# Performance work log

Measured on AMD Instinct MI355X. Metric: run time of the kernel, lower is better.

## Reference

```python
import jax, jax.numpy as jnp
import numpy as np

H, RANK, BATCH, T = 1024, 4, 128, 256


def setup_inputs() -> dict:
    key = jax.random.key(0)
    ks = jax.random.split(key, 6)
    s = 1.0 / np.sqrt(H)  # glorot-ish scale for params
    return {
        "x": jax.random.normal(ks[0], (BATCH, T, H), jnp.float32),
        "h0": jnp.zeros((BATCH, H), jnp.float32),
        "d": jax.random.normal(ks[1], (H,), jnp.float32) * s,
        "L": jax.random.normal(ks[2], (H, RANK), jnp.float32) * s,
        "R": jax.random.normal(ks[3], (RANK, H), jnp.float32) * s,
        "B": jax.random.normal(ks[4], (H, H), jnp.float32) * s,
    }


def reference(x, h0, d, L, R, B):
    # Input projection B.T @ x_t for all steps at once (one big GEMM):
    # (B.T @ x)_i = sum_j B[j,i] x[j]  ->  x @ B
    xB = jnp.einsum("bth,hk->btk", x, B)  # [batch, T, H]

    def step(h, u):  # h: [batch, H], u: [batch, H]
        # diagonal + rank-4 low-rank update: d*h + L @ (R @ h) + B.T @ x
        low_rank = (h @ R.T) @ L.T  # [batch, H]
        h = jnp.tanh(d * h + low_rank + u)
        return h, h

    _, hs = jax.lax.scan(step, h0, jnp.swapaxes(xB, 0, 1))  # hs: [T, batch, H]
    return jnp.swapaxes(hs, 0, 1)  # [batch, T, H]
```

## Files before the change

### kernel.cpp

```cpp
#include <hip/hip_runtime.h>
#include <hip/hip_bf16.h>

#define H_DIM  1024
#define RANK_  4
#define BATCH_ 128
#define TSTEPS 256
#define M_DIM  (BATCH_ * TSTEPS)

typedef __bf16 bf16x8 __attribute__((ext_vector_type(8)));
typedef float  floatx4 __attribute__((ext_vector_type(4)));
typedef unsigned short ushortx8 __attribute__((ext_vector_type(8)));

__device__ __forceinline__ unsigned short f2bf(float f) {
    unsigned u = __float_as_uint(f);
    u += 0x7FFFu + ((u >> 16) & 1u);
    return (unsigned short)(u >> 16);
}

#define NXB ((M_DIM * H_DIM) / (256 * 8))

__global__ __launch_bounds__(256) void cvt_fused_kernel(const float* __restrict__ x,
                                                        unsigned short* __restrict__ xb,
                                                        const float* __restrict__ B,
                                                        unsigned short* __restrict__ Bt) {
    __shared__ float tl[32][33];
    const int bid = blockIdx.x;
    if (bid < NXB) {
        size_t i = ((size_t)bid * 256 + threadIdx.x) * 8;
        float4 v0 = *(const float4*)(x + i);
        float4 v1 = *(const float4*)(x + i + 4);
        ushortx8 o;
        o[0] = f2bf(v0.x); o[1] = f2bf(v0.y); o[2] = f2bf(v0.z); o[3] = f2bf(v0.w);
        o[4] = f2bf(v1.x); o[5] = f2bf(v1.y); o[6] = f2bf(v1.z); o[7] = f2bf(v1.w);
        *(ushortx8*)(xb + i) = o;
    } else {
        const int t = bid - NXB;
        int tx = threadIdx.x & 31, ty = threadIdx.x >> 5;
        int k0 = (t >> 5) * 32, n0 = (t & 31) * 32;
#pragma unroll
        for (int j = 0; j < 4; ++j)
            tl[ty + 8 * j][tx] = B[(size_t)(k0 + ty + 8 * j) * H_DIM + n0 + tx];
        __syncthreads();
#pragma unroll
        for (int j = 0; j < 4; ++j)
            Bt[(size_t)(n0 + ty + 8 * j) * H_DIM + k0 + tx] = f2bf(tl[tx][ty + 8 * j]);
    }
}


#define BM 256
#define BN 256
#define BKK 64
#define KTILES (H_DIM / BKK)

#define GLD(srcptr, dstptr)                                          \
    __builtin_amdgcn_global_load_lds(                                \
        (const __attribute__((address_space(1))) void*)(srcptr),     \
        (__attribute__((address_space(3))) void*)(dstptr), 16, 0, 0)

#define STAGE_A(buf, hf, kt) do {                                                     \
    GLD(aS0 + (size_t)(hf) * (128 * H_DIM) + (kt) * BKK, &lds[buf][0][hf][dst0]);     \
    GLD(aS1 + (size_t)(hf) * (128 * H_DIM) + (kt) * BKK, &lds[buf][0][hf][dst1]);     \
} while (0)

#define STAGE_B(buf, hf, kt) do {                                                     \
    GLD(bS0 + (size_t)(hf) * (128 * H_DIM) + (kt) * BKK, &lds[buf][1][hf][dst0]);     \
    GLD(bS1 + (size_t)(hf) * (128 * H_DIM) + (kt) * BKK, &lds[buf][1][hf][dst1]);     \
} while (0)

#define MFMA_PHASE(q)                                                                                         \
    _Pragma("unroll")                                                                                         \
    for (int fc = 0; fc < 4; ++fc) {                                                                          \
        acc[2*(q)][fc]   = __builtin_amdgcn_mfma_f32_16x16x32_bf16(a00, bfr[fc][0], acc[2*(q)][fc], 0, 0, 0);   \
        acc[2*(q)][fc]   = __builtin_amdgcn_mfma_f32_16x16x32_bf16(a01, bfr[fc][1], acc[2*(q)][fc], 0, 0, 0);   \
        acc[2*(q)+1][fc] = __builtin_amdgcn_mfma_f32_16x16x32_bf16(a10, bfr[fc][0], acc[2*(q)+1][fc], 0, 0, 0); \
        acc[2*(q)+1][fc] = __builtin_amdgcn_mfma_f32_16x16x32_bf16(a11, bfr[fc][1], acc[2*(q)+1][fc], 0, 0, 0); \
    }

#define PHASE(q, STAGE_STMT, TAIL_STMT) {                                      \
        bf16x8 a00 = *(const bf16x8*)(Ah + (2*(q))     * 1024 + aRow + cs0);   \
        bf16x8 a01 = *(const bf16x8*)(Ah + (2*(q))     * 1024 + aRow + cs1);   \
        bf16x8 a10 = *(const bf16x8*)(Ah + (2*(q) + 1) * 1024 + aRow + cs0);   \
        bf16x8 a11 = *(const bf16x8*)(Ah + (2*(q) + 1) * 1024 + aRow + cs1);   \
        STAGE_STMT;                                                            \
        __builtin_amdgcn_s_barrier();                                          \
        asm volatile("s_waitcnt lgkmcnt(0)" ::: "memory");                     \
        __builtin_amdgcn_s_setprio(1);                                         \
        MFMA_PHASE(q);                                                         \
        __builtin_amdgcn_s_setprio(0);                                         \
        TAIL_STMT;                                                             \
        __builtin_amdgcn_s_barrier();                                          \
    }

__global__ __launch_bounds__(512, 2) void gemm_bf16_256(const unsigned short* __restrict__ A,
                                                        const unsigned short* __restrict__ Bt,
                                                        float* __restrict__ C) {
    __shared__ unsigned short lds[2][2][2][8192];

    const int tid = threadIdx.x;
    const int l   = tid & 63;
    const int w   = tid >> 6;
    const int wr  = w >> 2;
    const int wc  = w & 3;

    const int bid = blockIdx.x;
    const int lt  = (bid & 7) * 64 + (bid >> 3);
    const int m0  = (lt >> 2) * BM;
    const int n0  = (lt & 3)  * BN;

    const int p0row = (w * 2 + 0) * 8 + (l >> 3);
    const int p1row = (w * 2 + 1) * 8 + (l >> 3);
    const int gcol  = ((l & 7) ^ (l >> 3)) * 8;
    const int dst0  = (w * 2 + 0) * 512;
    const int dst1  = (w * 2 + 1) * 512;
    const unsigned short* aS0 = A  + (size_t)(m0 + p0row) * H_DIM + gcol;
    const unsigned short* aS1 = A  + (size_t)(m0 + p1row) * H_DIM + gcol;
    const unsigned short* bS0 = Bt + (size_t)(n0 + p0row) * H_DIM + gcol;
    const unsigned short* bS1 = Bt + (size_t)(n0 + p1row) * H_DIM + gcol;

    const int aRow = (l & 15) * 64;
    const int cs0  = (((l >> 4) + 0) ^ (l & 7)) * 8;
    const int cs1  = (((l >> 4) + 4) ^ (l & 7)) * 8;

    floatx4 acc[8][4];
#pragma unroll
    for (int i = 0; i < 8; ++i)
#pragma unroll
        for (int j = 0; j < 4; ++j) acc[i][j] = (floatx4){0.f, 0.f, 0.f, 0.f};

    STAGE_B(0, 0, 0); STAGE_B(0, 1, 0); STAGE_A(0, 0, 0); STAGE_A(0, 1, 0);
    STAGE_B(1, 0, 1); STAGE_B(1, 1, 1); STAGE_A(1, 0, 1);
    asm volatile("s_waitcnt vmcnt(6)" ::: "memory");
    __builtin_amdgcn_s_barrier();

    for (int kt = 0; kt < KTILES; ++kt) {
        const int buf = kt & 1;
        const unsigned short* Ah = &lds[buf][0][wr][0];
        const unsigned short* Bh = &lds[buf][1][wc >> 1][(wc & 1) * 4096];
        bf16x8 bfr[4][2];

        {
            bf16x8 a00 = *(const bf16x8*)(Ah + 0 * 1024 + aRow + cs0);
            bf16x8 a01 = *(const bf16x8*)(Ah + 0 * 1024 + aRow + cs1);
            bf16x8 a10 = *(const bf16x8*)(Ah + 1 * 1024 + aRow + cs0);
            bf16x8 a11 = *(const bf16x8*)(Ah + 1 * 1024 + aRow + cs1);
#pragma unroll
            for (int fc = 0; fc < 4; ++fc) {
                bfr[fc][0] = *(const bf16x8*)(Bh + fc * 1024 + aRow + cs0);
                bfr[fc][1] = *(const bf16x8*)(Bh + fc * 1024 + aRow + cs1);
            }
            if (kt + 1 < KTILES) STAGE_A(buf ^ 1, 1, kt + 1);
            __builtin_amdgcn_s_barrier();
            asm volatile("s_waitcnt lgkmcnt(0)" ::: "memory");
            __builtin_amdgcn_s_setprio(1);
            MFMA_PHASE(0);
            __builtin_amdgcn_s_setprio(0);
            __builtin_amdgcn_s_barrier();
        }
        PHASE(1, if (kt + 2 < KTILES) STAGE_B(buf, 0, kt + 2), );
        PHASE(2, if (kt + 2 < KTILES) STAGE_B(buf, 1, kt + 2), );
        PHASE(3, if (kt + 2 < KTILES) STAGE_A(buf, 0, kt + 2),
              if (kt < KTILES - 2) { asm volatile("s_waitcnt vmcnt(6)" ::: "memory"); }
              else if (kt == KTILES - 2) { asm volatile("s_waitcnt vmcnt(0)" ::: "memory"); });
    }

    const int cr = (l >> 4) * 4;
    const int cc = l & 15;
#pragma unroll
    for (int fr = 0; fr < 8; ++fr)
#pragma unroll
        for (int fc = 0; fc < 4; ++fc) {
            size_t base = (size_t)(m0 + wr * 128 + fr * 16 + cr) * H_DIM
                        + (n0 + wc * 64 + fc * 16 + cc);
#pragma unroll
            for (int r = 0; r < 4; ++r)
                C[base + (size_t)r * H_DIM] = acc[fr][fc][r];
        }
}

__global__ __launch_bounds__(256) void gemm_fp32_fallback(const float* __restrict__ A,
                                                          const float* __restrict__ B,
                                                          float* __restrict__ C) {
    __shared__ float As[64][20];
    __shared__ float Bs[16][68];
    const int tid = threadIdx.x;
    const int bm = blockIdx.x >> 4, bn = blockIdx.x & 15;
    const int m0 = bm * 64, n0 = bn * 64;
    const int tx = (tid & 15) * 4, ty = (tid >> 4) * 4;
    float acc[4][4];
#pragma unroll
    for (int i = 0; i < 4; ++i)
#pragma unroll
        for (int j = 0; j < 4; ++j) acc[i][j] = 0.f;

    for (int kk = 0; kk < H_DIM; kk += 16) {
        float4 av = *(const float4*)(A + (size_t)(m0 + (tid >> 2)) * H_DIM + kk + (tid & 3) * 4);
        float4 bv = *(const float4*)(B + (size_t)(kk + (tid >> 4)) * H_DIM + n0 + (tid & 15) * 4);
        __syncthreads();
        *(float4*)&As[tid >> 2][(tid & 3) * 4] = av;
        *(float4*)&Bs[tid >> 4][(tid & 15) * 4] = bv;
        __syncthreads();
#pragma unroll
        for (int k = 0; k < 16; ++k) {
            float a_[4], b_[4];
#pragma unroll
            for (int i = 0; i < 4; ++i) a_[i] = As[ty + i][k];
#pragma unroll
            for (int j = 0; j < 4; ++j) b_[j] = Bs[k][tx + j];
#pragma unroll
            for (int i = 0; i < 4; ++i)
#pragma unroll
                for (int j = 0; j < 4; ++j) acc[i][j] += a_[i] * b_[j];
        }
    }
#pragma unroll
    for (int i = 0; i < 4; ++i)
#pragma unroll
        for (int j = 0; j < 4; ++j)
            C[(size_t)(m0 + ty + i) * H_DIM + n0 + tx + j] = acc[i][j];
}


__device__ __forceinline__ float tanh_fast(float x) {
    float ax = fabsf(x);
    float e  = __expf(-2.0f * ax);
    float t  = (1.0f - e) * __builtin_amdgcn_rcpf(1.0f + e);
    return copysignf(t, x);
}

__device__ __forceinline__ void barrier_lds_only() {
    asm volatile("s_waitcnt lgkmcnt(0)\n\ts_barrier" ::: "memory");
}

template <int CTRL, int RMASK>
__device__ __forceinline__ float dpp_add(float x) {
    int v = __builtin_amdgcn_update_dpp(0, __float_as_int(x), CTRL, RMASK, 0xf, true);
    return x + __int_as_float(v);
}
__device__ __forceinline__ float wave_sum64(float x) {
    x = dpp_add<0x111, 0xf>(x);
    x = dpp_add<0x112, 0xf>(x);
    x = dpp_add<0x114, 0xf>(x);
    x = dpp_add<0x118, 0xf>(x);
    x = dpp_add<0x142, 0xa>(x);
    x = dpp_add<0x143, 0xc>(x);
    return x;
}

__global__ __launch_bounds__(256) void scan_kernel(const float* __restrict__ h0,
                                                   const float* __restrict__ d,
                                                   const float* __restrict__ Lm,
                                                   const float* __restrict__ Rm,
                                                   float* __restrict__ io) {
    const int b = blockIdx.x, tid = threadIdx.x;
    const int lane = tid & 63, wv = tid >> 6;
    const int e = tid * 4;

    float4 dv4 = *(const float4*)(d + e);
    float dd[4] = {dv4.x, dv4.y, dv4.z, dv4.w};
    float4 hv4 = *(const float4*)(h0 + (size_t)b * H_DIM + e);
    float h[4] = {hv4.x, hv4.y, hv4.z, hv4.w};

    float Lv[4][4], Rv[4][4];
#pragma unroll
    for (int i = 0; i < 4; ++i) {
        float4 t = *(const float4*)(Lm + (size_t)(e + i) * RANK_);
        Lv[i][0] = t.x; Lv[i][1] = t.y; Lv[i][2] = t.z; Lv[i][3] = t.w;
    }
#pragma unroll
    for (int j = 0; j < 4; ++j) {
        float4 t = *(const float4*)(Rm + (size_t)j * H_DIM + e);
        Rv[j][0] = t.x; Rv[j][1] = t.y; Rv[j][2] = t.z; Rv[j][3] = t.w;
    }

    float* iob = io + (size_t)b * TSTEPS * H_DIM + e;
    __shared__ float red[2][4][4];

    float4 u[4];
#pragma unroll
    for (int s = 0; s < 4; ++s) u[s] = *(const float4*)(iob + (size_t)s * H_DIM);

    for (int t = 0; t < TSTEPS; t += 4) {
#pragma unroll
        for (int s = 0; s < 4; ++s) {
            const int tt = t + s;
            float pr[4];
#pragma unroll
            for (int j = 0; j < 4; ++j)
                pr[j] = Rv[j][0] * h[0] + Rv[j][1] * h[1] + Rv[j][2] * h[2] + Rv[j][3] * h[3];
#pragma unroll
            for (int j = 0; j < 4; ++j) pr[j] = wave_sum64(pr[j]);
            if (lane == 63) {
                float4 w; w.x = pr[0]; w.y = pr[1]; w.z = pr[2]; w.w = pr[3];
                *(float4*)&red[s & 1][wv][0] = w;
            }
            float a_[4];
#pragma unroll
            for (int i = 0; i < 4; ++i) a_[i] = fmaf(dd[i], h[i], (&u[s].x)[i]);
            barrier_lds_only();
            float4 r0 = *(const float4*)&red[s & 1][0][0];
            float4 r1 = *(const float4*)&red[s & 1][1][0];
            float4 r2 = *(const float4*)&red[s & 1][2][0];
            float4 r3 = *(const float4*)&red[s & 1][3][0];
            float r[4] = {r0.x + r1.x + r2.x + r3.x, r0.y + r1.y + r2.y + r3.y,
                          r0.z + r1.z + r2.z + r3.z, r0.w + r1.w + r2.w + r3.w};

#pragma unroll
            for (int i = 0; i < 4; ++i) {
                float a = a_[i] + Lv[i][0] * r[0] + Lv[i][1] * r[1]
                                + Lv[i][2] * r[2] + Lv[i][3] * r[3];
                h[i] = tanh_fast(a);
            }
            float4 o; o.x = h[0]; o.y = h[1]; o.z = h[2]; o.w = h[3];
            *(float4*)(iob + (size_t)tt * H_DIM) = o;
            if (tt + 4 < TSTEPS) u[s] = *(const float4*)(iob + (size_t)(tt + 4) * H_DIM);
        }
    }
}


extern "C" void kernel_launch(void* const* d_in, const int* in_sizes, int n_in,
                              void* d_out, int out_size, void* d_ws, size_t ws_size,
                              hipStream_t stream) {
    const float* x  = (const float*)d_in[0];
    const float* h0 = (const float*)d_in[1];
    const float* dd = (const float*)d_in[2];
    const float* L  = (const float*)d_in[3];
    const float* R  = (const float*)d_in[4];
    const float* B  = (const float*)d_in[5];
    float* out = (float*)d_out;

    const size_t need = (size_t)M_DIM * H_DIM * sizeof(unsigned short)
                      + (size_t)H_DIM * H_DIM * sizeof(unsigned short);
    if (ws_size >= need) {
        unsigned short* xb = (unsigned short*)d_ws;
        unsigned short* Bt = xb + (size_t)M_DIM * H_DIM;
        cvt_fused_kernel<<<NXB + 1024, 256, 0, stream>>>(x, xb, B, Bt);
        gemm_bf16_256<<<(M_DIM / BM) * (H_DIM / BN), 512, 0, stream>>>(xb, Bt, out);
    } else {
        gemm_fp32_fallback<<<(M_DIM / 64) * (H_DIM / 64), 256, 0, stream>>>(x, B, out);
    }
    scan_kernel<<<BATCH_, 256, 0, stream>>>(h0, dd, L, R, out);
}
```

Baseline: 392.3 us.

## Run recurrent scan with one wave per batch row, removing LDS barrier

Restructures the scan kernel so each batch row is handled by a single 64-lane wave, each lane owning 16 hidden elements. The cross-wave LDS reduction and workgroup barrier become a wave-level DPP reduction plus a readlane broadcast, and the prefetch depth drops from 4 to 2 steps. This removes per-step barrier and LDS latency from the serial critical path, but each lane does four times more work per step and only 128 waves run across the GPU, so per-step latency may grow and register pressure rises.

```diff
diff --git a/kernel.cpp b/kernel.cpp
--- a/kernel.cpp
+++ b/kernel.cpp
@@ -228,10 +228,6 @@
     return copysignf(t, x);
 }
 
-__device__ __forceinline__ void barrier_lds_only() {
-    asm volatile("s_waitcnt lgkmcnt(0)\n\ts_barrier" ::: "memory");
-}
-
 template <int CTRL, int RMASK>
 __device__ __forceinline__ float dpp_add(float x) {
     int v = __builtin_amdgcn_update_dpp(0, __float_as_int(x), CTRL, RMASK, 0xf, true);
@@ -247,74 +243,90 @@
     return x;
 }
 
-__global__ __launch_bounds__(256) void scan_kernel(const float* __restrict__ h0,
-                                                   const float* __restrict__ d,
-                                                   const float* __restrict__ Lm,
-                                                   const float* __restrict__ Rm,
-                                                   float* __restrict__ io) {
-    const int b = blockIdx.x, tid = threadIdx.x;
-    const int lane = tid & 63, wv = tid >> 6;
-    const int e = tid * 4;
-
-    float4 dv4 = *(const float4*)(d + e);
-    float dd[4] = {dv4.x, dv4.y, dv4.z, dv4.w};
-    float4 hv4 = *(const float4*)(h0 + (size_t)b * H_DIM + e);
-    float h[4] = {hv4.x, hv4.y, hv4.z, hv4.w};
-
-    float Lv[4][4], Rv[4][4];
-#pragma unroll
-    for (int i = 0; i < 4; ++i) {
-        float4 t = *(const float4*)(Lm + (size_t)(e + i) * RANK_);
-        Lv[i][0] = t.x; Lv[i][1] = t.y; Lv[i][2] = t.z; Lv[i][3] = t.w;
-    }
-#pragma unroll
-    for (int j = 0; j < 4; ++j) {
-        float4 t = *(const float4*)(Rm + (size_t)j * H_DIM + e);
-        Rv[j][0] = t.x; Rv[j][1] = t.y; Rv[j][2] = t.z; Rv[j][3] = t.w;
-    }
-
-    float* iob = io + (size_t)b * TSTEPS * H_DIM + e;
-    __shared__ float red[2][4][4];
-
-    float4 u[4];
-#pragma unroll
-    for (int s = 0; s < 4; ++s) u[s] = *(const float4*)(iob + (size_t)s * H_DIM);
-
-    for (int t = 0; t < TSTEPS; t += 4) {
-#pragma unroll
-        for (int s = 0; s < 4; ++s) {
-            const int tt = t + s;
-            float pr[4];
-#pragma unroll
-            for (int j = 0; j < 4; ++j)
-                pr[j] = Rv[j][0] * h[0] + Rv[j][1] * h[1] + Rv[j][2] * h[2] + Rv[j][3] * h[3];
-#pragma unroll
-            for (int j = 0; j < 4; ++j) pr[j] = wave_sum64(pr[j]);
-            if (lane == 63) {
-                float4 w; w.x = pr[0]; w.y = pr[1]; w.z = pr[2]; w.w = pr[3];
-                *(float4*)&red[s & 1][wv][0] = w;
-            }
-            float a_[4];
-#pragma unroll
-            for (int i = 0; i < 4; ++i) a_[i] = fmaf(dd[i], h[i], (&u[s].x)[i]);
-            barrier_lds_only();
-            float4 r0 = *(const float4*)&red[s & 1][0][0];
-            float4 r1 = *(const float4*)&red[s & 1][1][0];
-            float4 r2 = *(const float4*)&red[s & 1][2][0];
-            float4 r3 = *(const float4*)&red[s & 1][3][0];
-            float r[4] = {r0.x + r1.x + r2.x + r3.x, r0.y + r1.y + r2.y + r3.y,
-                          r0.z + r1.z + r2.z + r3.z, r0.w + r1.w + r2.w + r3.w};
-
-#pragma unroll
-            for (int i = 0; i < 4; ++i) {
-                float a = a_[i] + Lv[i][0] * r[0] + Lv[i][1] * r[1]
-                                + Lv[i][2] * r[2] + Lv[i][3] * r[3];
-                h[i] = tanh_fast(a);
-            }
-            float4 o; o.x = h[0]; o.y = h[1]; o.z = h[2]; o.w = h[3];
-            *(float4*)(iob + (size_t)tt * H_DIM) = o;
-            if (tt + 4 < TSTEPS) u[s] = *(const float4*)(iob + (size_t)(tt + 4) * H_DIM);
-        }
+#define SCAN_STEP(U, tt) {                                                          \
+    float pra[4], prb[4];                                                           \
+    _Pragma("unroll")                                                               \
+    for (int j = 0; j < 4; ++j) {                                                   \
+        pra[j] = Rv[j][0][0] * h[0][0];                                             \
+        prb[j] = Rv[j][2][0] * h[2][0];                                             \
+        _Pragma("unroll")                                                           \
+        for (int c = 1; c < 4; ++c) {                                               \
+            pra[j] = fmaf(Rv[j][0][c], h[0][c], pra[j]);                            \
+            prb[j] = fmaf(Rv[j][2][c], h[2][c], prb[j]);                            \
+        }                                                                           \
+        _Pragma("unroll")                                                           \
+        for (int c = 0; c < 4; ++c) {                                               \
+            pra[j] = fmaf(Rv[j][1][c], h[1][c], pra[j]);                            \
+            prb[j] = fmaf(Rv[j][3][c], h[3][c], prb[j]);                            \
+        }                                                                           \
+    }                                                                               \
+    float r[4];                                                                     \
+    _Pragma("unroll")                                                               \
+    for (int j = 0; j < 4; ++j) {                                                   \
+        float s_ = wave_sum64(pra[j] + prb[j]);                                     \
+        r[j] = __int_as_float(__builtin_amdgcn_readlane(__float_as_int(s_), 63));   \
+    }                                                                               \
+    _Pragma("unroll")                                                               \
+    for (int q = 0; q < 4; ++q) {                                                   \
+        float4 o;                                                                   \
+        _Pragma("unroll")                                                           \
+        for (int c = 0; c < 4; ++c) {                                               \
+            float a = fmaf(dd[q][c], h[q][c], (&U[q].x)[c]);                        \
+            a = fmaf(Lv[q][c][0], r[0], a);                                         \
+            a = fmaf(Lv[q][c][1], r[1], a);                                         \
+            a = fmaf(Lv[q][c][2], r[2], a);                                         \
+            a = fmaf(Lv[q][c][3], r[3], a);                                         \
+            h[q][c] = tanh_fast(a);                                                 \
+            (&o.x)[c] = h[q][c];                                                    \
+        }                                                                           \
+        *(float4*)(iob + (size_t)(tt) * H_DIM + q * 256) = o;                       \
+    }                                                                               \
+    if ((tt) + 2 < TSTEPS) {                                                        \
+        _Pragma("unroll")                                                           \
+        for (int q = 0; q < 4; ++q)                                                 \
+            U[q] = *(const float4*)(iob + (size_t)((tt) + 2) * H_DIM + q * 256);    \
+    }                                                                               \
+}
+
+__global__ __launch_bounds__(64, 1) void scan_kernel(const float* __restrict__ h0,
+                                                     const float* __restrict__ d,
+                                                     const float* __restrict__ Lm,
+                                                     const float* __restrict__ Rm,
+                                                     float* __restrict__ io) {
+    const int b = blockIdx.x, l = threadIdx.x;
+
+    float h[4][4], dd[4][4], Lv[4][4][4], Rv[4][4][4];
+#pragma unroll
+    for (int q = 0; q < 4; ++q) {
+        float4 hv = *(const float4*)(h0 + (size_t)b * H_DIM + q * 256 + l * 4);
+        h[q][0] = hv.x; h[q][1] = hv.y; h[q][2] = hv.z; h[q][3] = hv.w;
+        float4 dv = *(const float4*)(d + q * 256 + l * 4);
+        dd[q][0] = dv.x; dd[q][1] = dv.y; dd[q][2] = dv.z; dd[q][3] = dv.w;
+#pragma unroll
+        for (int c = 0; c < 4; ++c) {
+            float4 lv = *(const float4*)(Lm + (size_t)(q * 256 + l * 4 + c) * RANK_);
+            Lv[q][c][0] = lv.x; Lv[q][c][1] = lv.y; Lv[q][c][2] = lv.z; Lv[q][c][3] = lv.w;
+        }
+    }
+#pragma unroll
+    for (int j = 0; j < 4; ++j)
+#pragma unroll
+        for (int q = 0; q < 4; ++q) {
+            float4 rv = *(const float4*)(Rm + (size_t)j * H_DIM + q * 256 + l * 4);
+            Rv[j][q][0] = rv.x; Rv[j][q][1] = rv.y; Rv[j][q][2] = rv.z; Rv[j][q][3] = rv.w;
+        }
+
+    float* iob = io + (size_t)b * TSTEPS * H_DIM + l * 4;
+
+    float4 u0[4], u1[4];
+#pragma unroll
+    for (int q = 0; q < 4; ++q) u0[q] = *(const float4*)(iob + 0 * H_DIM + q * 256);
+#pragma unroll
+    for (int q = 0; q < 4; ++q) u1[q] = *(const float4*)(iob + 1 * H_DIM + q * 256);
+
+    for (int t = 0; t < TSTEPS; t += 2) {
+        SCAN_STEP(u0, t);
+        SCAN_STEP(u1, t + 1);
     }
 }
 
@@ -340,5 +352,5 @@
     } else {
         gemm_fp32_fallback<<<(M_DIM / 64) * (H_DIM / 64), 256, 0, stream>>>(x, B, out);
     }
-    scan_kernel<<<BATCH_, 256, 0, stream>>>(h0, dd, L, R, out);
-}
+    scan_kernel<<<BATCH_, 64, 0, stream>>>(h0, dd, L, R, out);
+}
```

New measurement: 438.5 us. 11.8% more time.
